# Kernel optimization log

Hardware: AMD Instinct MI355X
Metric: run time of the kernel (lower is better)

## Reference

```python
import jax, jax.numpy as jnp
import numpy as np

D_MODEL = 1024
N_HEADS = 16
D_KEY = D_MODEL // N_HEADS
NEG = -1e9


def setup_inputs() -> dict:
    key = jax.random.key(0)
    ks = jax.random.split(key, 10)
    B, S = 4, 2048
    s = 0.02
    query = jax.random.normal(ks[0], (B, S, D_MODEL), dtype=jnp.float32)
    # causal mask: 1 where attend allowed, 0 where masked (masked_fill(mask==0, -1e9))
    mask = jnp.tril(jnp.ones((S, S), dtype=jnp.int32))[None, None]
    Wq = jax.random.normal(ks[1], (D_MODEL, D_MODEL), dtype=jnp.float32) * s
    bq = jax.random.normal(ks[2], (D_MODEL,), dtype=jnp.float32) * s
    Wk = jax.random.normal(ks[3], (D_MODEL, D_MODEL), dtype=jnp.float32) * s
    bk = jax.random.normal(ks[4], (D_MODEL,), dtype=jnp.float32) * s
    Wv = jax.random.normal(ks[5], (D_MODEL, D_MODEL), dtype=jnp.float32) * s
    bv = jax.random.normal(ks[6], (D_MODEL,), dtype=jnp.float32) * s
    Wo = jax.random.normal(ks[7], (D_MODEL, D_MODEL), dtype=jnp.float32) * s
    bo = jax.random.normal(ks[8], (D_MODEL,), dtype=jnp.float32) * s
    return {"query": query, "mask": mask, "Wq": Wq, "bq": bq, "Wk": Wk,
            "bk": bk, "Wv": Wv, "bv": bv, "Wo": Wo, "bo": bo}


def _split_heads(x):
    B, S, _ = x.shape
    return x.reshape(B, S, N_HEADS, D_KEY).transpose(0, 2, 1, 3)  # [B,H,S,Dk]


def reference(query, mask, Wq, bq, Wk, bk, Wv, bv, Wo, bo):
    B, S, _ = query.shape
    # torch Linear: x @ W^T + b
    q = _split_heads(query @ Wq.T + bq)
    k = _split_heads(query @ Wk.T + bk)  # self-attention: key_value is None
    v = _split_heads(query @ Wv.T + bv)
    scores = jnp.einsum('bhqd,bhkd->bhqk', q, k) / jnp.sqrt(jnp.float32(D_KEY))
    scores = jnp.where(mask == 0, jnp.float32(NEG), scores)
    weights = jax.nn.softmax(scores, axis=-1)  # dropout=0 (eval)
    attn = jnp.einsum('bhqk,bhkd->bhqd', weights, v)
    merged = attn.transpose(0, 2, 1, 3).reshape(B, S, D_MODEL)
    return merged @ Wo.T + bo
```

## Files before the change

### kernel.cpp

```cpp
#include <hip/hip_runtime.h>
#include <hip/hip_bf16.h>

typedef __attribute__((ext_vector_type(8))) short bf16x8;
typedef __attribute__((ext_vector_type(4))) float f32x4;
typedef __attribute__((ext_vector_type(16))) float f32x16;
typedef __attribute__((ext_vector_type(2))) unsigned int u32x2;

__device__ __forceinline__ float fexp2(float x) { return __builtin_amdgcn_exp2f(x); }

__device__ __forceinline__ ushort f2bf(float x) {
    union { float f; unsigned u; } c; c.f = x;
    unsigned r = c.u + 0x7fff + ((c.u >> 16) & 1);
    return (ushort)(r >> 16);
}

__device__ __forceinline__ unsigned cvtpk(float lo, float hi) {
    unsigned r;
    asm("v_cvt_pk_bf16_f32 %0, %1, %2" : "=v"(r) : "v"(lo), "v"(hi));
    return r;
}

__device__ __forceinline__ void gload16(const void* g, void* l) {
    __builtin_amdgcn_global_load_lds((const __attribute__((address_space(1))) void*)g,
                                     (__attribute__((address_space(3))) void*)l, 16, 0, 0);
}

__device__ __forceinline__ void blockbar() {
    asm volatile("" ::: "memory");
    __builtin_amdgcn_s_barrier();
    asm volatile("" ::: "memory");
}

__global__ void cvt_all(const float* __restrict__ X, const float* __restrict__ wa,
                        const float* __restrict__ wb, const float* __restrict__ wc,
                        const float* __restrict__ wd,
                        ushort* __restrict__ oX, ushort* __restrict__ oWcat,
                        ushort* __restrict__ oWo) {
    const int NX4 = 2097152;
    const int NW4 = 262144;
    const int TOT = NX4 + 4 * NW4;
    int i = blockIdx.x * blockDim.x + threadIdx.x;
    int stride = gridDim.x * blockDim.x;
    for (; i < TOT; i += stride) {
        const float* src; ushort4* dst; int local;
        if (i < NX4) { src = X; local = i; dst = (ushort4*)oX; }
        else {
            int j = i - NX4, sel = j >> 18; local = j & (NW4 - 1);
            src = (sel == 0) ? wa : (sel == 1) ? wb : (sel == 2) ? wc : wd;
            dst = (sel < 3) ? (ushort4*)oWcat + sel * NW4 : (ushort4*)oWo;
        }
        float4 v = ((const float4*)src)[local];
        ushort4 o;
        o.x = f2bf(v.x); o.y = f2bf(v.y); o.z = f2bf(v.z); o.w = f2bf(v.w);
        dst[local] = o;
    }
}

template<int MODE>
__global__ __launch_bounds__(512, 4)
void gemm_bk32(const ushort* __restrict__ A, const ushort* __restrict__ Bt,
               const float* __restrict__ bias0, const float* __restrict__ bias1,
               const float* __restrict__ bias2,
               ushort* __restrict__ outb, float* __restrict__ outf,
               int M, int N, int K) {
    __shared__ ushort lds[24576];
    const int t = threadIdx.x, lane = t & 63, w = t >> 6;
    const int wm = w >> 1, wn = w & 1;
    const int l15 = lane & 15, lg = lane >> 4;

    const int nbx = N >> 7;
    const int nwg = nbx * (M >> 8);
    const int bid = blockIdx.y * nbx + blockIdx.x;
    const int swz = (bid & 7) * (nwg >> 3) + (bid >> 3);
    const int m0 = (swz / nbx) * 256, n0 = (swz % nbx) * 128;

    const int rA0 = t >> 2, pcb = t & 3;
    const int rA1 = rA0 + 128;
    const int gA0 = pcb ^ ((rA0 >> 1) & 3);
    const int gA1 = pcb ^ ((rA1 >> 1) & 3);
    const ushort* srcA0 = A + (size_t)(m0 + rA0) * K + gA0 * 8;
    const ushort* srcA1 = A + (size_t)(m0 + rA1) * K + gA1 * 8;
    const ushort* srcB  = Bt + (size_t)(n0 + rA0) * K + gA0 * 8;

#define STAGE(ST, KT) { \
    gload16(srcA0 + (KT) * 32, &lds[(ST) * 12288 + t * 8]); \
    gload16(srcA1 + (KT) * 32, &lds[(ST) * 12288 + 4096 + t * 8]); \
    gload16(srcB  + (KT) * 32, &lds[(ST) * 12288 + 8192 + t * 8]); }

    f32x4 acc[4][4] = {};
    const int NT = K >> 5;

    STAGE(0, 0); STAGE(1, 1);

    for (int kt = 0; kt < NT; ++kt) {
        if (kt < NT - 1) asm volatile("s_waitcnt vmcnt(3)" ::: "memory");
        else             asm volatile("s_waitcnt vmcnt(0)" ::: "memory");
        blockbar();

        const ushort* stg = &lds[(kt & 1) * 12288];
        bf16x8 af[4], bfr[4];
#pragma unroll
        for (int mi = 0; mi < 4; mi++) {
            int row = wm * 64 + mi * 16 + l15;
            af[mi] = *(const bf16x8*)&stg[row * 32 + ((lg ^ ((row >> 1) & 3)) << 3)];
        }
#pragma unroll
        for (int ni = 0; ni < 4; ni++) {
            int row = wn * 64 + ni * 16 + l15;
            bfr[ni] = *(const bf16x8*)&stg[8192 + row * 32 + ((lg ^ ((row >> 1) & 3)) << 3)];
        }

        __builtin_amdgcn_s_setprio(1);
#pragma unroll
        for (int mi = 0; mi < 4; mi++)
#pragma unroll
            for (int ni = 0; ni < 4; ni++)
                acc[mi][ni] = __builtin_amdgcn_mfma_f32_16x16x32_bf16(af[mi], bfr[ni], acc[mi][ni], 0, 0, 0);
        __builtin_amdgcn_s_setprio(0);

        asm volatile("s_waitcnt lgkmcnt(0)" ::: "memory");
        blockbar();
        if (kt + 2 < NT) STAGE((kt & 1), kt + 2);
    }
#undef STAGE

#pragma unroll
    for (int mi = 0; mi < 4; mi++)
#pragma unroll
        for (int ni = 0; ni < 4; ni++)
#pragma unroll
            for (int r = 0; r < 4; r++) {
                int gm = m0 + wm * 64 + mi * 16 + lg * 4 + r;
                int gn = n0 + wn * 64 + ni * 16 + l15;
                if (MODE == 0) {
                    const float* bp = (gn < 1024) ? bias0 : ((gn < 2048) ? bias1 : bias2);
                    float v = acc[mi][ni][r] + bp[gn & 1023];
                    if (gn < 1024) v *= 0.18033688011f;
                    int proj = gn >> 10, nn = gn & 1023;
                    int h = nn >> 6, d = nn & 63;
                    int b = gm >> 11, s = gm & 2047;
                    outb[(size_t)proj * 8388608 + ((((size_t)b << 4) + h) * 2048 + s) * 64 + d] = f2bf(v);
                } else {
                    outf[(size_t)gm * N + gn] = acc[mi][ni][r] + bias0[gn];
                }
            }
}

template<int MODE>
__global__ __launch_bounds__(512, 2)
void gemm_p2(const ushort* __restrict__ A, const ushort* __restrict__ Bt,
             const float* __restrict__ bias0, const float* __restrict__ bias1,
             const float* __restrict__ bias2,
             ushort* __restrict__ outb, float* __restrict__ outf,
             int M, int N, int K) {
    __shared__ ushort lds[49152];
    const int t = threadIdx.x, lane = t & 63, w = t >> 6;
    const int wm = w >> 1, wn = w & 1;
    const int l15 = lane & 15, lg = lane >> 4;
    const int sw7 = l15 & 7;

    const int nbx = N >> 7;
    const int nwg = nbx * (M >> 8);
    const int bid = blockIdx.y * nbx + blockIdx.x;
    const int swz = (bid & 7) * (nwg >> 3) + (bid >> 3);
    const int m0 = (swz / nbx) * 256, n0 = (swz % nbx) * 128;

    const int srow = lane >> 3;
    const int gcb = (lane & 7) ^ srow;
    const ushort* gsrc[6];
#pragma unroll
    for (int s = 0; s < 4; s++)
        gsrc[s] = A + (size_t)(m0 + s * 64 + w * 8 + srow) * K + gcb * 8;
#pragma unroll
    for (int s = 0; s < 2; s++)
        gsrc[4 + s] = Bt + (size_t)(n0 + s * 64 + w * 8 + srow) * K + gcb * 8;

#define STAGE(ST, KT) { \
    ushort* dst = &lds[(ST) * 24576 + w * 512]; \
    gload16(gsrc[0] + (KT) * 64, dst); \
    gload16(gsrc[1] + (KT) * 64, dst + 4096); \
    gload16(gsrc[2] + (KT) * 64, dst + 8192); \
    gload16(gsrc[3] + (KT) * 64, dst + 12288); \
    gload16(gsrc[4] + (KT) * 64, dst + 16384); \
    gload16(gsrc[5] + (KT) * 64, dst + 20480); }

    f32x4 acc[4][4] = {};
    const int NT = K >> 6;

    STAGE(0, 0); STAGE(1, 1);

    for (int kt = 0; kt < NT; ++kt) {
        if (kt < NT - 1) asm volatile("s_waitcnt vmcnt(6)" ::: "memory");
        else             asm volatile("s_waitcnt vmcnt(0)" ::: "memory");
        blockbar();

        const ushort* stg = &lds[(kt & 1) * 24576];
        bf16x8 a0[4], b0[4], a1[4], b1[4];
#pragma unroll
        for (int mi = 0; mi < 4; mi++) {
            int row = wm * 64 + mi * 16 + l15;
            a0[mi] = *(const bf16x8*)&stg[row * 64 + ((lg ^ sw7) << 3)];
            a1[mi] = *(const bf16x8*)&stg[row * 64 + (((4 + lg) ^ sw7) << 3)];
        }
#pragma unroll
        for (int ni = 0; ni < 4; ni++) {
            int row = wn * 64 + ni * 16 + l15;
            b0[ni] = *(const bf16x8*)&stg[16384 + row * 64 + ((lg ^ sw7) << 3)];
            b1[ni] = *(const bf16x8*)&stg[16384 + row * 64 + (((4 + lg) ^ sw7) << 3)];
        }

        __builtin_amdgcn_s_setprio(1);
#pragma unroll
        for (int mi = 0; mi < 4; mi++)
#pragma unroll
            for (int ni = 0; ni < 4; ni++)
                acc[mi][ni] = __builtin_amdgcn_mfma_f32_16x16x32_bf16(a0[mi], b0[ni], acc[mi][ni], 0, 0, 0);
        __builtin_amdgcn_s_setprio(0);

        asm volatile("s_waitcnt lgkmcnt(0)" ::: "memory");
        blockbar();
        if (kt + 2 < NT) STAGE((kt & 1), kt + 2);

        __builtin_amdgcn_s_setprio(1);
#pragma unroll
        for (int mi = 0; mi < 4; mi++)
#pragma unroll
            for (int ni = 0; ni < 4; ni++)
                acc[mi][ni] = __builtin_amdgcn_mfma_f32_16x16x32_bf16(a1[mi], b1[ni], acc[mi][ni], 0, 0, 0);
        __builtin_amdgcn_s_setprio(0);
    }
#undef STAGE

#pragma unroll
    for (int mi = 0; mi < 4; mi++)
#pragma unroll
        for (int ni = 0; ni < 4; ni++)
#pragma unroll
            for (int r = 0; r < 4; r++) {
                int gm = m0 + wm * 64 + mi * 16 + lg * 4 + r;
                int gn = n0 + wn * 64 + ni * 16 + l15;
                if (MODE == 0) {
                    const float* bp = (gn < 1024) ? bias0 : ((gn < 2048) ? bias1 : bias2);
                    float v = acc[mi][ni][r] + bp[gn & 1023];
                    if (gn < 1024) v *= 0.18033688011f;
                    int proj = gn >> 10, nn = gn & 1023;
                    int h = nn >> 6, d = nn & 63;
                    int b = gm >> 11, s = gm & 2047;
                    outb[(size_t)proj * 8388608 + ((((size_t)b << 4) + h) * 2048 + s) * 64 + d] = f2bf(v);
                } else {
                    outf[(size_t)gm * N + gn] = acc[mi][ni][r] + bias0[gn];
                }
            }
}

__global__ __launch_bounds__(256, 4)
void attn_fwd(const ushort* __restrict__ Qb, const ushort* __restrict__ Kb,
              const ushort* __restrict__ Vb, ushort* __restrict__ Ab) {
    constexpr int S = 2048;
    __shared__ ushort lds[16384];

    const int bid = blockIdx.x;
    const int qt = 15 - (bid >> 6);
    const int bh = bid & 63;
    const int b = bh >> 4, h = bh & 15;
    const ushort* Qp = Qb + (size_t)bh * S * 64;
    const ushort* Kp = Kb + (size_t)bh * S * 64;
    const ushort* Vp = Vb + (size_t)bh * S * 64;

    const int t = threadIdx.x, lane = t & 63, w = t >> 6;
    const int l15 = lane & 15, l31 = lane & 31, hi = lane >> 5, g = lane >> 4;

    int koff[2], voff[2];
#pragma unroll
    for (int i = 0; i < 2; i++) {
        int row = (w * 2 + i) * 8 + (lane >> 3);
        int gg = (lane & 7) ^ ((row ^ (row >> 3)) & 7);
        koff[i] = row * 64 + gg * 8;
    }
#pragma unroll
    for (int it = 0; it < 2; it++) {
        int T = (it * 4 + w) * 64 + lane;
        int kvb = T >> 5, db = (T >> 3) & 3, kvr = (T >> 1) & 3, dh = T & 1;
        voff[it] = (kvb * 4 + kvr) * 64 + db * 16 + dh * 8;
    }
    const unsigned vtbase = (unsigned)(uintptr_t)&lds[8192]
                          + (hi << 10) + ((g & 1) << 7) + (l15 << 3);

    auto stage = [&](int phase, int k0) {
#pragma unroll
        for (int i = 0; i < 2; i++)
            gload16(Kp + (size_t)k0 * 64 + koff[i], &lds[(phase << 12) + ((w * 2 + i) << 9)]);
#pragma unroll
        for (int it = 0; it < 2; it++)
            gload16(Vp + (size_t)k0 * 64 + voff[it], &lds[8192 + (phase << 12) + (((it << 2) + w) << 9)]);
    };

    const int fb = qt * 128 + w * 32;
    const int nt = 2 * qt + 2;

    bf16x8 qf[4];
#pragma unroll
    for (int kc = 0; kc < 4; kc++)
        qf[kc] = *(const bf16x8*)&Qp[(size_t)(fb + l31) * 64 + kc * 16 + hi * 8];

    float m = -3e38f, ls = 0.f;
    f32x16 O0 = {}, O1 = {};

    stage(0, 0);

    for (int tile = 0; tile < nt; tile++) {
        const int phase = tile & 1;
        const int k0 = tile * 64;
        asm volatile("s_waitcnt vmcnt(0)" ::: "memory");
        blockbar();
        if (tile + 1 < nt) stage(phase ^ 1, (tile + 1) * 64);

        if (k0 <= fb + 31) {
            const ushort* Kc = &lds[phase << 12];
            f32x16 s0 = {}, s1 = {};
            {
                bf16x8 kf[4];
#pragma unroll
                for (int kc = 0; kc < 4; kc++) {
                    int row = l31;
                    int sw = (row ^ (row >> 3)) & 7;
                    kf[kc] = *(const bf16x8*)&Kc[row * 64 + (((kc * 2 + hi) ^ sw) << 3)];
                }
                __builtin_amdgcn_s_setprio(1);
#pragma unroll
                for (int kc = 0; kc < 4; kc++)
                    s0 = __builtin_amdgcn_mfma_f32_32x32x16_bf16(kf[kc], qf[kc], s0, 0, 0, 0);
                __builtin_amdgcn_s_setprio(0);
            }
            {
                bf16x8 kf[4];
#pragma unroll
                for (int kc = 0; kc < 4; kc++) {
                    int row = 32 + l31;
                    int sw = (row ^ (row >> 3)) & 7;
                    kf[kc] = *(const bf16x8*)&Kc[row * 64 + (((kc * 2 + hi) ^ sw) << 3)];
                }
                __builtin_amdgcn_s_setprio(1);
#pragma unroll
                for (int kc = 0; kc < 4; kc++)
                    s1 = __builtin_amdgcn_mfma_f32_32x32x16_bf16(kf[kc], qf[kc], s1, 0, 0, 0);
                __builtin_amdgcn_s_setprio(0);
            }

            const bool diag = (k0 + 63 > fb);
            if (diag) {
                const int rel = fb + l31 - k0 - 4 * hi;
#pragma unroll
                for (int r = 0; r < 16; r++) {
                    int kvc = (r & 3) + 8 * (r >> 2);
                    if (kvc > rel)      s0[r] = -1e30f;
                    if (kvc + 32 > rel) s1[r] = -1e30f;
                }
            }
            float pv[32];
#pragma unroll
            for (int r = 0; r < 16; r++) { pv[r] = s0[r]; pv[16 + r] = s1[r]; }
            float mx[16];
#pragma unroll
            for (int i = 0; i < 16; i++) mx[i] = fmaxf(pv[i], pv[i + 16]);
#pragma unroll
            for (int sgap = 8; sgap >= 1; sgap >>= 1)
#pragma unroll
                for (int i = 0; i < sgap; i++) mx[i] = fmaxf(mx[i], mx[i + sgap]);
            float pmax = fmaxf(mx[0], __shfl_xor(mx[0], 32));

            if (!__all(pmax <= m + 8.f)) {
                float mnew = fmaxf(m, pmax);
                float a = fexp2(m - mnew);
                ls *= a;
                float ar[16];
#pragma unroll
                for (int r = 0; r < 16; r++)
                    ar[r] = __shfl(a, (r & 3) + 8 * (r >> 2) + 4 * hi, 32);
#pragma unroll
                for (int r = 0; r < 16; r++) { O0[r] *= ar[r]; O1[r] *= ar[r]; }
                m = mnew;
            }
#pragma unroll
            for (int i = 0; i < 32; i++) pv[i] = fexp2(pv[i] - m);
            float sm[16];
#pragma unroll
            for (int i = 0; i < 16; i++) sm[i] = pv[i] + pv[i + 16];
#pragma unroll
            for (int sgap = 8; sgap >= 1; sgap >>= 1)
#pragma unroll
                for (int i = 0; i < sgap; i++) sm[i] += sm[i + sgap];
            ls += sm[0] + __shfl_xor(sm[0], 32);

            union PAu { bf16x8 v; unsigned wd[4]; } PA[4];
#pragma unroll
            for (int ks = 0; ks < 4; ks++)
#pragma unroll
                for (int i = 0; i < 2; i++) {
                    unsigned xw = cvtpk(pv[8 * ks + 2 * i], pv[8 * ks + 2 * i + 1]);
                    unsigned yw = cvtpk(pv[8 * ks + 2 * i + 4], pv[8 * ks + 2 * i + 5]);
                    asm("v_permlane32_swap_b32 %0, %1" : "+v"(xw), "+v"(yw));
                    PA[ks].wd[i] = xw; PA[ks].wd[2 + i] = yw;
                }

            const unsigned vtb = vtbase + (phase << 13);
            u32x2 vb[16];
#define TRR(idx, OFFSTR) asm volatile("ds_read_b64_tr_b16 %0, %1 offset:" OFFSTR : "=v"(vb[idx]) : "v"(vtb))
            TRR(0, "0");    TRR(1, "512");  TRR(2, "2048"); TRR(3, "2560");
            TRR(4, "4096"); TRR(5, "4608"); TRR(6, "6144"); TRR(7, "6656");
            TRR(8, "256");  TRR(9, "768");  TRR(10, "2304"); TRR(11, "2816");
            TRR(12, "4352"); TRR(13, "4864"); TRR(14, "6400"); TRR(15, "6912");
#undef TRR
            union FragU { bf16x8 v; u32x2 hh[2]; };
            asm volatile("s_waitcnt lgkmcnt(8)" ::: "memory");
            __builtin_amdgcn_sched_barrier(0);
            __builtin_amdgcn_s_setprio(1);
#pragma unroll
            for (int ks = 0; ks < 4; ks++) {
                FragU f; f.hh[0] = vb[ks * 2]; f.hh[1] = vb[ks * 2 + 1];
                O0 = __builtin_amdgcn_mfma_f32_32x32x16_bf16(PA[ks].v, f.v, O0, 0, 0, 0);
            }
            __builtin_amdgcn_s_setprio(0);
            asm volatile("s_waitcnt lgkmcnt(0)" ::: "memory");
            __builtin_amdgcn_sched_barrier(0);
            __builtin_amdgcn_s_setprio(1);
#pragma unroll
            for (int ks = 0; ks < 4; ks++) {
                FragU f; f.hh[0] = vb[8 + ks * 2]; f.hh[1] = vb[8 + ks * 2 + 1];
                O1 = __builtin_amdgcn_mfma_f32_32x32x16_bf16(PA[ks].v, f.v, O1, 0, 0, 0);
            }
            __builtin_amdgcn_s_setprio(0);
        }
    }

    float inv[16];
#pragma unroll
    for (int r = 0; r < 16; r++)
        inv[r] = __builtin_amdgcn_rcpf(__shfl(ls, (r & 3) + 8 * (r >> 2) + 4 * hi, 32));
#pragma unroll
    for (int r = 0; r < 16; r++) {
        int q = fb + (r & 3) + 8 * (r >> 2) + 4 * hi;
        size_t base = ((size_t)b * 2048 + q) * 1024 + h * 64;
        Ab[base + l31]      = f2bf(O0[r] * inv[r]);
        Ab[base + 32 + l31] = f2bf(O1[r] * inv[r]);
    }
}

extern "C" void kernel_launch(void* const* d_in, const int* in_sizes, int n_in,
                              void* d_out, int out_size, void* d_ws, size_t ws_size,
                              hipStream_t stream) {
    const float* query = (const float*)d_in[0];
    const float* Wq = (const float*)d_in[2];
    const float* bq = (const float*)d_in[3];
    const float* Wk = (const float*)d_in[4];
    const float* bk = (const float*)d_in[5];
    const float* Wv = (const float*)d_in[6];
    const float* bv = (const float*)d_in[7];
    const float* Wo = (const float*)d_in[8];
    const float* bo = (const float*)d_in[9];
    float* out = (float*)d_out;

    char* ws = (char*)d_ws;
    const size_t SZ_X = 8192ull * 1024 * 2;
    const size_t SZ_W = 1024ull * 1024 * 2;
    ushort* Xb   = (ushort*)(ws);
    ushort* Wcat = (ushort*)(ws + SZ_X);
    ushort* Wob  = (ushort*)(ws + SZ_X + 3 * SZ_W);
    ushort* QKVb = (ushort*)(ws + SZ_X + 4 * SZ_W);
    ushort* Ab   = (ushort*)(ws + 4 * SZ_X + 4 * SZ_W);

    cvt_all<<<2048, 256, 0, stream>>>(query, Wq, Wk, Wv, Wo, Xb, Wcat, Wob);

    gemm_bk32<0><<<dim3(3072 / 128, 8192 / 256), 512, 0, stream>>>(
        Xb, Wcat, bq, bk, bv, QKVb, nullptr, 8192, 3072, 1024);

    attn_fwd<<<1024, 256, 0, stream>>>(QKVb, QKVb + 8388608, QKVb + 2 * 8388608, Ab);

    gemm_p2<1><<<dim3(1024 / 128, 8192 / 256), 512, 0, stream>>>(
        Ab, Wob, bo, nullptr, nullptr, nullptr, out, 8192, 1024, 1024);
}
```

Measured before the change: 154.4 us.

## Use smaller 128x128 tiles with BK32 for the output projection GEMM

```diff
diff --git a/kernel.cpp b/kernel.cpp
--- a/kernel.cpp
+++ b/kernel.cpp
@@ -56,13 +56,11 @@
     }
 }
 
-template<int MODE>
 __global__ __launch_bounds__(512, 4)
-void gemm_bk32(const ushort* __restrict__ A, const ushort* __restrict__ Bt,
-               const float* __restrict__ bias0, const float* __restrict__ bias1,
-               const float* __restrict__ bias2,
-               ushort* __restrict__ outb, float* __restrict__ outf,
-               int M, int N, int K) {
+void gemm_qkv(const ushort* __restrict__ A, const ushort* __restrict__ Bt,
+              const float* __restrict__ bias0, const float* __restrict__ bias1,
+              const float* __restrict__ bias2,
+              ushort* __restrict__ outb, int M, int N, int K) {
     __shared__ ushort lds[24576];
     const int t = threadIdx.x, lane = t & 63, w = t >> 6;
     const int wm = w >> 1, wn = w & 1;
@@ -132,81 +130,67 @@
             for (int r = 0; r < 4; r++) {
                 int gm = m0 + wm * 64 + mi * 16 + lg * 4 + r;
                 int gn = n0 + wn * 64 + ni * 16 + l15;
-                if (MODE == 0) {
-                    const float* bp = (gn < 1024) ? bias0 : ((gn < 2048) ? bias1 : bias2);
-                    float v = acc[mi][ni][r] + bp[gn & 1023];
-                    if (gn < 1024) v *= 0.18033688011f;
-                    int proj = gn >> 10, nn = gn & 1023;
-                    int h = nn >> 6, d = nn & 63;
-                    int b = gm >> 11, s = gm & 2047;
-                    outb[(size_t)proj * 8388608 + ((((size_t)b << 4) + h) * 2048 + s) * 64 + d] = f2bf(v);
-                } else {
-                    outf[(size_t)gm * N + gn] = acc[mi][ni][r] + bias0[gn];
-                }
-            }
-}
-
-template<int MODE>
-__global__ __launch_bounds__(512, 2)
-void gemm_p2(const ushort* __restrict__ A, const ushort* __restrict__ Bt,
-             const float* __restrict__ bias0, const float* __restrict__ bias1,
-             const float* __restrict__ bias2,
-             ushort* __restrict__ outb, float* __restrict__ outf,
-             int M, int N, int K) {
-    __shared__ ushort lds[49152];
+                const float* bp = (gn < 1024) ? bias0 : ((gn < 2048) ? bias1 : bias2);
+                float v = acc[mi][ni][r] + bp[gn & 1023];
+                if (gn < 1024) v *= 0.18033688011f;
+                int proj = gn >> 10, nn = gn & 1023;
+                int h = nn >> 6, d = nn & 63;
+                int b = gm >> 11, s = gm & 2047;
+                outb[(size_t)proj * 8388608 + ((((size_t)b << 4) + h) * 2048 + s) * 64 + d] = f2bf(v);
+            }
+}
+
+__global__ __launch_bounds__(256, 8)
+void gemm_out(const ushort* __restrict__ A, const ushort* __restrict__ Bt,
+              const float* __restrict__ bias0,
+              float* __restrict__ outf, int M, int N, int K) {
+    __shared__ ushort lds[16384];
     const int t = threadIdx.x, lane = t & 63, w = t >> 6;
     const int wm = w >> 1, wn = w & 1;
     const int l15 = lane & 15, lg = lane >> 4;
-    const int sw7 = l15 & 7;
 
     const int nbx = N >> 7;
-    const int nwg = nbx * (M >> 8);
+    const int nwg = nbx * (M >> 7);
     const int bid = blockIdx.y * nbx + blockIdx.x;
     const int swz = (bid & 7) * (nwg >> 3) + (bid >> 3);
-    const int m0 = (swz / nbx) * 256, n0 = (swz % nbx) * 128;
-
-    const int srow = lane >> 3;
-    const int gcb = (lane & 7) ^ srow;
-    const ushort* gsrc[6];
-#pragma unroll
-    for (int s = 0; s < 4; s++)
-        gsrc[s] = A + (size_t)(m0 + s * 64 + w * 8 + srow) * K + gcb * 8;
-#pragma unroll
-    for (int s = 0; s < 2; s++)
-        gsrc[4 + s] = Bt + (size_t)(n0 + s * 64 + w * 8 + srow) * K + gcb * 8;
+    const int m0 = (swz / nbx) * 128, n0 = (swz % nbx) * 128;
+
+    const int r0 = t >> 2, pcb = t & 3;
+    const int r1 = r0 + 64;
+    const int g0 = pcb ^ ((r0 >> 1) & 3);
+    const int g1 = pcb ^ ((r1 >> 1) & 3);
+    const ushort* srcA0 = A + (size_t)(m0 + r0) * K + g0 * 8;
+    const ushort* srcA1 = A + (size_t)(m0 + r1) * K + g1 * 8;
+    const ushort* srcB0 = Bt + (size_t)(n0 + r0) * K + g0 * 8;
+    const ushort* srcB1 = Bt + (size_t)(n0 + r1) * K + g1 * 8;
 
 #define STAGE(ST, KT) { \
-    ushort* dst = &lds[(ST) * 24576 + w * 512]; \
-    gload16(gsrc[0] + (KT) * 64, dst); \
-    gload16(gsrc[1] + (KT) * 64, dst + 4096); \
-    gload16(gsrc[2] + (KT) * 64, dst + 8192); \
-    gload16(gsrc[3] + (KT) * 64, dst + 12288); \
-    gload16(gsrc[4] + (KT) * 64, dst + 16384); \
-    gload16(gsrc[5] + (KT) * 64, dst + 20480); }
+    gload16(srcA0 + (KT) * 32, &lds[(ST) * 8192 + t * 8]); \
+    gload16(srcA1 + (KT) * 32, &lds[(ST) * 8192 + 2048 + t * 8]); \
+    gload16(srcB0 + (KT) * 32, &lds[(ST) * 8192 + 4096 + t * 8]); \
+    gload16(srcB1 + (KT) * 32, &lds[(ST) * 8192 + 6144 + t * 8]); }
 
     f32x4 acc[4][4] = {};
-    const int NT = K >> 6;
+    const int NT = K >> 5;
 
     STAGE(0, 0); STAGE(1, 1);
 
     for (int kt = 0; kt < NT; ++kt) {
-        if (kt < NT - 1) asm volatile("s_waitcnt vmcnt(6)" ::: "memory");
+        if (kt < NT - 1) asm volatile("s_waitcnt vmcnt(4)" ::: "memory");
         else             asm volatile("s_waitcnt vmcnt(0)" ::: "memory");
         blockbar();
 
-        const ushort* stg = &lds[(kt & 1) * 24576];
-        bf16x8 a0[4], b0[4], a1[4], b1[4];
+        const ushort* stg = &lds[(kt & 1) * 8192];
+        bf16x8 af[4], bfr[4];
 #pragma unroll
         for (int mi = 0; mi < 4; mi++) {
             int row = wm * 64 + mi * 16 + l15;
-            a0[mi] = *(const bf16x8*)&stg[row * 64 + ((lg ^ sw7) << 3)];
-            a1[mi] = *(const bf16x8*)&stg[row * 64 + (((4 + lg) ^ sw7) << 3)];
+            af[mi] = *(const bf16x8*)&stg[row * 32 + ((lg ^ ((row >> 1) & 3)) << 3)];
         }
 #pragma unroll
         for (int ni = 0; ni < 4; ni++) {
             int row = wn * 64 + ni * 16 + l15;
-            b0[ni] = *(const bf16x8*)&stg[16384 + row * 64 + ((lg ^ sw7) << 3)];
-            b1[ni] = *(const bf16x8*)&stg[16384 + row * 64 + (((4 + lg) ^ sw7) << 3)];
+            bfr[ni] = *(const bf16x8*)&stg[4096 + row * 32 + ((lg ^ ((row >> 1) & 3)) << 3)];
         }
 
         __builtin_amdgcn_s_setprio(1);
@@ -214,20 +198,12 @@
         for (int mi = 0; mi < 4; mi++)
 #pragma unroll
             for (int ni = 0; ni < 4; ni++)
-                acc[mi][ni] = __builtin_amdgcn_mfma_f32_16x16x32_bf16(a0[mi], b0[ni], acc[mi][ni], 0, 0, 0);
+                acc[mi][ni] = __builtin_amdgcn_mfma_f32_16x16x32_bf16(af[mi], bfr[ni], acc[mi][ni], 0, 0, 0);
         __builtin_amdgcn_s_setprio(0);
 
         asm volatile("s_waitcnt lgkmcnt(0)" ::: "memory");
         blockbar();
         if (kt + 2 < NT) STAGE((kt & 1), kt + 2);
-
-        __builtin_amdgcn_s_setprio(1);
-#pragma unroll
-        for (int mi = 0; mi < 4; mi++)
-#pragma unroll
-            for (int ni = 0; ni < 4; ni++)
-                acc[mi][ni] = __builtin_amdgcn_mfma_f32_16x16x32_bf16(a1[mi], b1[ni], acc[mi][ni], 0, 0, 0);
-        __builtin_amdgcn_s_setprio(0);
     }
 #undef STAGE
 
@@ -239,17 +215,7 @@
             for (int r = 0; r < 4; r++) {
                 int gm = m0 + wm * 64 + mi * 16 + lg * 4 + r;
                 int gn = n0 + wn * 64 + ni * 16 + l15;
-                if (MODE == 0) {
-                    const float* bp = (gn < 1024) ? bias0 : ((gn < 2048) ? bias1 : bias2);
-                    float v = acc[mi][ni][r] + bp[gn & 1023];
-                    if (gn < 1024) v *= 0.18033688011f;
-                    int proj = gn >> 10, nn = gn & 1023;
-                    int h = nn >> 6, d = nn & 63;
-                    int b = gm >> 11, s = gm & 2047;
-                    outb[(size_t)proj * 8388608 + ((((size_t)b << 4) + h) * 2048 + s) * 64 + d] = f2bf(v);
-                } else {
-                    outf[(size_t)gm * N + gn] = acc[mi][ni][r] + bias0[gn];
-                }
+                outf[(size_t)gm * N + gn] = acc[mi][ni][r] + bias0[gn];
             }
 }
 
@@ -471,11 +437,11 @@
 
     cvt_all<<<2048, 256, 0, stream>>>(query, Wq, Wk, Wv, Wo, Xb, Wcat, Wob);
 
-    gemm_bk32<0><<<dim3(3072 / 128, 8192 / 256), 512, 0, stream>>>(
-        Xb, Wcat, bq, bk, bv, QKVb, nullptr, 8192, 3072, 1024);
+    gemm_qkv<<<dim3(3072 / 128, 8192 / 256), 512, 0, stream>>>(
+        Xb, Wcat, bq, bk, bv, QKVb, 8192, 3072, 1024);
 
     attn_fwd<<<1024, 256, 0, stream>>>(QKVb, QKVb + 8388608, QKVb + 2 * 8388608, Ab);
 
-    gemm_p2<1><<<dim3(1024 / 128, 8192 / 256), 512, 0, stream>>>(
-        Ab, Wob, bo, nullptr, nullptr, nullptr, out, 8192, 1024, 1024);
-}
+    gemm_out<<<dim3(1024 / 128, 8192 / 128), 256, 0, stream>>>(
+        Ab, Wob, bo, out, 8192, 1024, 1024);
+}
```

New measurement: 155.9 us. No clear change (+1.0%).

## Load K tiles directly into registers with double-buffered prefetch in attention

Applied to the files above, without the earlier changes.

```diff
diff --git a/kernel.cpp b/kernel.cpp
--- a/kernel.cpp
+++ b/kernel.cpp
@@ -56,13 +56,11 @@
     }
 }
 
-template<int MODE>
 __global__ __launch_bounds__(512, 4)
-void gemm_bk32(const ushort* __restrict__ A, const ushort* __restrict__ Bt,
-               const float* __restrict__ bias0, const float* __restrict__ bias1,
-               const float* __restrict__ bias2,
-               ushort* __restrict__ outb, float* __restrict__ outf,
-               int M, int N, int K) {
+void gemm_qkv(const ushort* __restrict__ A, const ushort* __restrict__ Bt,
+              const float* __restrict__ bias0, const float* __restrict__ bias1,
+              const float* __restrict__ bias2,
+              ushort* __restrict__ outb, int M, int N, int K) {
     __shared__ ushort lds[24576];
     const int t = threadIdx.x, lane = t & 63, w = t >> 6;
     const int wm = w >> 1, wn = w & 1;
@@ -132,27 +130,20 @@
             for (int r = 0; r < 4; r++) {
                 int gm = m0 + wm * 64 + mi * 16 + lg * 4 + r;
                 int gn = n0 + wn * 64 + ni * 16 + l15;
-                if (MODE == 0) {
-                    const float* bp = (gn < 1024) ? bias0 : ((gn < 2048) ? bias1 : bias2);
-                    float v = acc[mi][ni][r] + bp[gn & 1023];
-                    if (gn < 1024) v *= 0.18033688011f;
-                    int proj = gn >> 10, nn = gn & 1023;
-                    int h = nn >> 6, d = nn & 63;
-                    int b = gm >> 11, s = gm & 2047;
-                    outb[(size_t)proj * 8388608 + ((((size_t)b << 4) + h) * 2048 + s) * 64 + d] = f2bf(v);
-                } else {
-                    outf[(size_t)gm * N + gn] = acc[mi][ni][r] + bias0[gn];
-                }
-            }
-}
-
-template<int MODE>
+                const float* bp = (gn < 1024) ? bias0 : ((gn < 2048) ? bias1 : bias2);
+                float v = acc[mi][ni][r] + bp[gn & 1023];
+                if (gn < 1024) v *= 0.18033688011f;
+                int proj = gn >> 10, nn = gn & 1023;
+                int h = nn >> 6, d = nn & 63;
+                int b = gm >> 11, s = gm & 2047;
+                outb[(size_t)proj * 8388608 + ((((size_t)b << 4) + h) * 2048 + s) * 64 + d] = f2bf(v);
+            }
+}
+
 __global__ __launch_bounds__(512, 2)
-void gemm_p2(const ushort* __restrict__ A, const ushort* __restrict__ Bt,
-             const float* __restrict__ bias0, const float* __restrict__ bias1,
-             const float* __restrict__ bias2,
-             ushort* __restrict__ outb, float* __restrict__ outf,
-             int M, int N, int K) {
+void gemm_outp(const ushort* __restrict__ A, const ushort* __restrict__ Bt,
+               const float* __restrict__ bias0,
+               float* __restrict__ outf, int M, int N, int K) {
     __shared__ ushort lds[49152];
     const int t = threadIdx.x, lane = t & 63, w = t >> 6;
     const int wm = w >> 1, wn = w & 1;
@@ -239,25 +230,15 @@
             for (int r = 0; r < 4; r++) {
                 int gm = m0 + wm * 64 + mi * 16 + lg * 4 + r;
                 int gn = n0 + wn * 64 + ni * 16 + l15;
-                if (MODE == 0) {
-                    const float* bp = (gn < 1024) ? bias0 : ((gn < 2048) ? bias1 : bias2);
-                    float v = acc[mi][ni][r] + bp[gn & 1023];
-                    if (gn < 1024) v *= 0.18033688011f;
-                    int proj = gn >> 10, nn = gn & 1023;
-                    int h = nn >> 6, d = nn & 63;
-                    int b = gm >> 11, s = gm & 2047;
-                    outb[(size_t)proj * 8388608 + ((((size_t)b << 4) + h) * 2048 + s) * 64 + d] = f2bf(v);
-                } else {
-                    outf[(size_t)gm * N + gn] = acc[mi][ni][r] + bias0[gn];
-                }
-            }
-}
-
-__global__ __launch_bounds__(256, 4)
+                outf[(size_t)gm * N + gn] = acc[mi][ni][r] + bias0[gn];
+            }
+}
+
+__global__ __launch_bounds__(256, 3)
 void attn_fwd(const ushort* __restrict__ Qb, const ushort* __restrict__ Kb,
               const ushort* __restrict__ Vb, ushort* __restrict__ Ab) {
     constexpr int S = 2048;
-    __shared__ ushort lds[16384];
+    __shared__ ushort lds[8192];
 
     const int bid = blockIdx.x;
     const int qt = 15 - (bid >> 6);
@@ -270,29 +251,28 @@
     const int t = threadIdx.x, lane = t & 63, w = t >> 6;
     const int l15 = lane & 15, l31 = lane & 31, hi = lane >> 5, g = lane >> 4;
 
-    int koff[2], voff[2];
-#pragma unroll
-    for (int i = 0; i < 2; i++) {
-        int row = (w * 2 + i) * 8 + (lane >> 3);
-        int gg = (lane & 7) ^ ((row ^ (row >> 3)) & 7);
-        koff[i] = row * 64 + gg * 8;
-    }
+    int voff[2];
 #pragma unroll
     for (int it = 0; it < 2; it++) {
         int T = (it * 4 + w) * 64 + lane;
         int kvb = T >> 5, db = (T >> 3) & 3, kvr = (T >> 1) & 3, dh = T & 1;
         voff[it] = (kvb * 4 + kvr) * 64 + db * 16 + dh * 8;
     }
-    const unsigned vtbase = (unsigned)(uintptr_t)&lds[8192]
+    const unsigned vtbase = (unsigned)(uintptr_t)&lds[0]
                           + (hi << 10) + ((g & 1) << 7) + (l15 << 3);
 
-    auto stage = [&](int phase, int k0) {
-#pragma unroll
-        for (int i = 0; i < 2; i++)
-            gload16(Kp + (size_t)k0 * 64 + koff[i], &lds[(phase << 12) + ((w * 2 + i) << 9)]);
+    auto stageV = [&](int phase, int k0) {
 #pragma unroll
         for (int it = 0; it < 2; it++)
-            gload16(Vp + (size_t)k0 * 64 + voff[it], &lds[8192 + (phase << 12) + (((it << 2) + w) << 9)]);
+            gload16(Vp + (size_t)k0 * 64 + voff[it], &lds[(phase << 12) + (((it << 2) + w) << 9)]);
+    };
+
+    auto loadK = [&](bf16x8 (&DL)[4], bf16x8 (&DH)[4], int kk0) {
+#pragma unroll
+        for (int kc = 0; kc < 4; kc++) {
+            DL[kc] = *(const bf16x8*)&Kp[(size_t)(kk0 + l31) * 64 + (kc * 2 + hi) * 8];
+            DH[kc] = *(const bf16x8*)&Kp[(size_t)(kk0 + 32 + l31) * 64 + (kc * 2 + hi) * 8];
+        }
     };
 
     const int fb = qt * 128 + w * 32;
@@ -306,46 +286,30 @@
     float m = -3e38f, ls = 0.f;
     f32x16 O0 = {}, O1 = {};
 
-    stage(0, 0);
-
-    for (int tile = 0; tile < nt; tile++) {
-        const int phase = tile & 1;
+    bf16x8 kAl[4], kAh[4], kBl[4], kBh[4];
+
+#define TRR(idx, OFFSTR) asm volatile("ds_read_b64_tr_b16 %0, %1 offset:" OFFSTR : "=v"(vb[idx]) : "v"(vtb))
+
+    auto body = [&](bf16x8 (&KL)[4], bf16x8 (&KH)[4], bf16x8 (&NKL)[4], bf16x8 (&NKH)[4],
+                    int phase, int tile) {
         const int k0 = tile * 64;
         asm volatile("s_waitcnt vmcnt(0)" ::: "memory");
         blockbar();
-        if (tile + 1 < nt) stage(phase ^ 1, (tile + 1) * 64);
+        if (tile + 1 < nt) stageV(phase ^ 1, (tile + 1) * 64);
 
         if (k0 <= fb + 31) {
-            const ushort* Kc = &lds[phase << 12];
             f32x16 s0 = {}, s1 = {};
-            {
-                bf16x8 kf[4];
-#pragma unroll
-                for (int kc = 0; kc < 4; kc++) {
-                    int row = l31;
-                    int sw = (row ^ (row >> 3)) & 7;
-                    kf[kc] = *(const bf16x8*)&Kc[row * 64 + (((kc * 2 + hi) ^ sw) << 3)];
-                }
-                __builtin_amdgcn_s_setprio(1);
-#pragma unroll
-                for (int kc = 0; kc < 4; kc++)
-                    s0 = __builtin_amdgcn_mfma_f32_32x32x16_bf16(kf[kc], qf[kc], s0, 0, 0, 0);
-                __builtin_amdgcn_s_setprio(0);
-            }
-            {
-                bf16x8 kf[4];
-#pragma unroll
-                for (int kc = 0; kc < 4; kc++) {
-                    int row = 32 + l31;
-                    int sw = (row ^ (row >> 3)) & 7;
-                    kf[kc] = *(const bf16x8*)&Kc[row * 64 + (((kc * 2 + hi) ^ sw) << 3)];
-                }
-                __builtin_amdgcn_s_setprio(1);
-#pragma unroll
-                for (int kc = 0; kc < 4; kc++)
-                    s1 = __builtin_amdgcn_mfma_f32_32x32x16_bf16(kf[kc], qf[kc], s1, 0, 0, 0);
-                __builtin_amdgcn_s_setprio(0);
-            }
+            __builtin_amdgcn_s_setprio(1);
+#pragma unroll
+            for (int kc = 0; kc < 4; kc++)
+                s0 = __builtin_amdgcn_mfma_f32_32x32x16_bf16(KL[kc], qf[kc], s0, 0, 0, 0);
+#pragma unroll
+            for (int kc = 0; kc < 4; kc++)
+                s1 = __builtin_amdgcn_mfma_f32_32x32x16_bf16(KH[kc], qf[kc], s1, 0, 0, 0);
+            __builtin_amdgcn_s_setprio(0);
+
+            if (tile + 1 < nt && (tile + 1) * 64 <= fb + 31)
+                loadK(NKL, NKH, (tile + 1) * 64);
 
             const bool diag = (k0 + 63 > fb);
             if (diag) {
@@ -404,34 +368,46 @@
                 }
 
             const unsigned vtb = vtbase + (phase << 13);
-            u32x2 vb[16];
-#define TRR(idx, OFFSTR) asm volatile("ds_read_b64_tr_b16 %0, %1 offset:" OFFSTR : "=v"(vb[idx]) : "v"(vtb))
-            TRR(0, "0");    TRR(1, "512");  TRR(2, "2048"); TRR(3, "2560");
-            TRR(4, "4096"); TRR(5, "4608"); TRR(6, "6144"); TRR(7, "6656");
-            TRR(8, "256");  TRR(9, "768");  TRR(10, "2304"); TRR(11, "2816");
-            TRR(12, "4352"); TRR(13, "4864"); TRR(14, "6400"); TRR(15, "6912");
+            union FragU { bf16x8 v; u32x2 hh[2]; };
+            {
+                u32x2 vb[8];
+                TRR(0, "0");    TRR(1, "512");  TRR(2, "2048"); TRR(3, "2560");
+                TRR(4, "4096"); TRR(5, "4608"); TRR(6, "6144"); TRR(7, "6656");
+                asm volatile("s_waitcnt lgkmcnt(0)" ::: "memory");
+                __builtin_amdgcn_sched_barrier(0);
+                __builtin_amdgcn_s_setprio(1);
+#pragma unroll
+                for (int ks = 0; ks < 4; ks++) {
+                    FragU f; f.hh[0] = vb[ks * 2]; f.hh[1] = vb[ks * 2 + 1];
+                    O0 = __builtin_amdgcn_mfma_f32_32x32x16_bf16(PA[ks].v, f.v, O0, 0, 0, 0);
+                }
+                __builtin_amdgcn_s_setprio(0);
+            }
+            {
+                u32x2 vb[8];
+                TRR(0, "256");  TRR(1, "768");  TRR(2, "2304"); TRR(3, "2816");
+                TRR(4, "4352"); TRR(5, "4864"); TRR(6, "6400"); TRR(7, "6912");
+                asm volatile("s_waitcnt lgkmcnt(0)" ::: "memory");
+                __builtin_amdgcn_sched_barrier(0);
+                __builtin_amdgcn_s_setprio(1);
+#pragma unroll
+                for (int ks = 0; ks < 4; ks++) {
+                    FragU f; f.hh[0] = vb[ks * 2]; f.hh[1] = vb[ks * 2 + 1];
+                    O1 = __builtin_amdgcn_mfma_f32_32x32x16_bf16(PA[ks].v, f.v, O1, 0, 0, 0);
+                }
+                __builtin_amdgcn_s_setprio(0);
+            }
+        }
+    };
+
+    loadK(kAl, kAh, 0);
+    stageV(0, 0);
+
+    for (int tp = 0; tp < nt; tp += 2) {
+        body(kAl, kAh, kBl, kBh, 0, tp);
+        body(kBl, kBh, kAl, kAh, 1, tp + 1);
+    }
 #undef TRR
-            union FragU { bf16x8 v; u32x2 hh[2]; };
-            asm volatile("s_waitcnt lgkmcnt(8)" ::: "memory");
-            __builtin_amdgcn_sched_barrier(0);
-            __builtin_amdgcn_s_setprio(1);
-#pragma unroll
-            for (int ks = 0; ks < 4; ks++) {
-                FragU f; f.hh[0] = vb[ks * 2]; f.hh[1] = vb[ks * 2 + 1];
-                O0 = __builtin_amdgcn_mfma_f32_32x32x16_bf16(PA[ks].v, f.v, O0, 0, 0, 0);
-            }
-            __builtin_amdgcn_s_setprio(0);
-            asm volatile("s_waitcnt lgkmcnt(0)" ::: "memory");
-            __builtin_amdgcn_sched_barrier(0);
-            __builtin_amdgcn_s_setprio(1);
-#pragma unroll
-            for (int ks = 0; ks < 4; ks++) {
-                FragU f; f.hh[0] = vb[8 + ks * 2]; f.hh[1] = vb[8 + ks * 2 + 1];
-                O1 = __builtin_amdgcn_mfma_f32_32x32x16_bf16(PA[ks].v, f.v, O1, 0, 0, 0);
-            }
-            __builtin_amdgcn_s_setprio(0);
-        }
-    }
 
     float inv[16];
 #pragma unroll
@@ -471,11 +447,11 @@
 
     cvt_all<<<2048, 256, 0, stream>>>(query, Wq, Wk, Wv, Wo, Xb, Wcat, Wob);
 
-    gemm_bk32<0><<<dim3(3072 / 128, 8192 / 256), 512, 0, stream>>>(
-        Xb, Wcat, bq, bk, bv, QKVb, nullptr, 8192, 3072, 1024);
+    gemm_qkv<<<dim3(3072 / 128, 8192 / 256), 512, 0, stream>>>(
+        Xb, Wcat, bq, bk, bv, QKVb, 8192, 3072, 1024);
 
     attn_fwd<<<1024, 256, 0, stream>>>(QKVb, QKVb + 8388608, QKVb + 2 * 8388608, Ab);
 
-    gemm_p2<1><<<dim3(1024 / 128, 8192 / 256), 512, 0, stream>>>(
-        Ab, Wob, bo, nullptr, nullptr, nullptr, out, 8192, 1024, 1024);
-}
+    gemm_outp<<<dim3(1024 / 128, 8192 / 256), 512, 0, stream>>>(
+        Ab, Wob, bo, out, 8192, 1024, 1024);
+}
```

Measured after the change: 200.9 us. 30.1% more time.
